# Performance work log

Measured on AMD Instinct MI355X. Metric: run time of the kernel, lower is better.

## Reference

```python
import jax, jax.numpy as jnp
import numpy as np

B, S, D = 16, 2048, 256
HEAD_SIZE = 256  # input_size // num_heads = 256 // 1
SCALE = HEAD_SIZE ** -0.5


def setup_inputs() -> dict:
    key = jax.random.key(0)
    ks = jax.random.split(key, 4)
    s = 1.0 / np.sqrt(D)  # typical linear init scale
    return {
        "x": jax.random.normal(ks[0], (B, S, D), dtype=jnp.float32),
        "Wq": jax.random.normal(ks[1], (D, D), dtype=jnp.float32) * s,
        "bq": jnp.zeros((D,), dtype=jnp.float32),
        "Wk": jax.random.normal(ks[2], (D, D), dtype=jnp.float32) * s,
        "bk": jnp.zeros((D,), dtype=jnp.float32),
        "Wv": jax.random.normal(ks[3], (D, D), dtype=jnp.float32) * s,
        "bv": jnp.zeros((D,), dtype=jnp.float32),
    }


def reference(x, Wq, bq, Wk, bk, Wv, bv):
    # Linear projections (torch Linear: x @ W.T + b)
    q = jnp.einsum("bsd,ed->bse", x, Wq) + bq
    k = jnp.einsum("bsd,ed->bse", x, Wk) + bk
    v = jnp.einsum("bsd,ed->bse", x, Wv) + bv
    # Full attention matrix [B, S, S], scaled by head_size^-0.5
    scores = jnp.einsum("bqd,bkd->bqk", q, k) * SCALE
    attn = jax.nn.softmax(scores, axis=-1)
    # dropout is identity in inference/reference mode
    out = jnp.einsum("bqk,bkd->bqd", attn, v)
    return out
```

## Files before the change

kernel.cpp:

```cpp
#include <hip/hip_runtime.h>
#include <hip/hip_bf16.h>
#include <stdint.h>

#define DEV __device__ __forceinline__

typedef __attribute__((ext_vector_type(8))) short bf16x8;
typedef __attribute__((ext_vector_type(4))) float f32x4;
typedef unsigned short u16;

DEV void gload_lds16(const void* g, void* l) {
    typedef const __attribute__((address_space(1))) unsigned int* gp_t;
    typedef __attribute__((address_space(3))) unsigned int* lp_t;
    __builtin_amdgcn_global_load_lds((gp_t)(uintptr_t)g, (lp_t)(uint32_t)(uintptr_t)l, 16, 0, 0);
}

DEV u16 f2bf(float x) {
    union { __hip_bfloat16 h; u16 u; } c;
    c.h = __float2bfloat16(x);
    return c.u;
}
DEV unsigned pack2bf(float a, float b) {
    return (unsigned)f2bf(a) | ((unsigned)f2bf(b) << 16);
}

__global__ void cast_kernel(const float* __restrict__ src, u16* __restrict__ dst, int n8) {
    int stride = gridDim.x * blockDim.x;
    for (int i = blockIdx.x * blockDim.x + threadIdx.x; i < n8; i += stride) {
        const float4* s = (const float4*)src + (size_t)i * 2;
        float4 a = s[0], b = s[1];
        union { u16 u[8]; uint4 v; } o;
        o.u[0] = f2bf(a.x); o.u[1] = f2bf(a.y); o.u[2] = f2bf(a.z); o.u[3] = f2bf(a.w);
        o.u[4] = f2bf(b.x); o.u[5] = f2bf(b.y); o.u[6] = f2bf(b.z); o.u[7] = f2bf(b.w);
        *((uint4*)dst + i) = o.v;
    }
}

DEV void gemm_body(const u16* A, const u16* Bw, const float* bias, int bias_row,
                   u16* out, int out_pitch)
{
    __shared__ char smA[16384];
    __shared__ char smB[16384];
    const int lane = threadIdx.x & 63;
    const int w    = threadIdx.x >> 6;
    const int wr   = w >> 1, wc = w & 1;
    const int l15  = lane & 15, lg = lane >> 4;

    f32x4 acc[4][4] = {};
    const char* ag = (const char*)A;
    const char* bg = (const char*)Bw;

    for (int kt = 0; kt < 4; ++kt) {
        __syncthreads();
        #pragma unroll
        for (int c = 0; c < 8; ++c) {
            int ch    = w * 8 + c;
            int loc   = ch & 15;
            int p     = loc * 1024 + lane * 16;
            int row   = p >> 7;
            int inner = (p & 127) ^ ((row & 7) << 4);
            const char* src = (ch < 16 ? ag : bg) + row * 512 + kt * 128 + inner;
            char* dst = (ch < 16 ? smA : smB) + loc * 1024;
            gload_lds16(src, dst);
        }
        __syncthreads();
        #pragma unroll
        for (int ks = 0; ks < 2; ++ks) {
            bf16x8 af[4], bfr[4];
            #pragma unroll
            for (int mi = 0; mi < 4; ++mi) {
                int row = wr * 64 + mi * 16 + l15;
                af[mi] = *(const bf16x8*)(smA + ((row * 128 + ks * 64 + lg * 16) ^ ((row & 7) << 4)));
            }
            #pragma unroll
            for (int ni = 0; ni < 4; ++ni) {
                int row = wc * 64 + ni * 16 + l15;
                bfr[ni] = *(const bf16x8*)(smB + ((row * 128 + ks * 64 + lg * 16) ^ ((row & 7) << 4)));
            }
            #pragma unroll
            for (int mi = 0; mi < 4; ++mi)
                #pragma unroll
                for (int ni = 0; ni < 4; ++ni)
                    acc[mi][ni] = __builtin_amdgcn_mfma_f32_16x16x32_bf16(af[mi], bfr[ni], acc[mi][ni], 0, 0, 0);
        }
    }
    #pragma unroll
    for (int mi = 0; mi < 4; ++mi) {
        #pragma unroll
        for (int ni = 0; ni < 4; ++ni) {
            int n_l  = wc * 64 + ni * 16 + l15;
            float bn = bias_row ? 0.f : bias[n_l];
            #pragma unroll
            for (int r = 0; r < 4; ++r) {
                int row  = wr * 64 + mi * 16 + lg * 4 + r;
                float bb = bias_row ? bias[row] : bn;
                out[(size_t)row * out_pitch + n_l] = f2bf(acc[mi][ni][r] + bb);
            }
        }
    }
}

__global__ __launch_bounds__(256) void proj_qk_kernel(
    const u16* xb, const u16* wqb, const u16* wkb,
    const float* bq, const float* bk, u16* Q, u16* K)
{
    int n0 = blockIdx.x * 128;
    int m0 = blockIdx.y * 128;
    bool isK = n0 >= 256;
    int  nl  = n0 & 255;
    gemm_body(xb + (size_t)m0 * 256, (isK ? wkb : wqb) + (size_t)nl * 256,
              (isK ? bk : bq) + nl, 0,
              (isK ? K : Q) + (size_t)m0 * 256 + nl, 256);
}

__global__ __launch_bounds__(256) void proj_v_kernel(
    const u16* wvb, const u16* xb, const float* bv, u16* Vt)
{
    int n0 = blockIdx.x * 128;
    int m0 = blockIdx.y * 128;
    gemm_body(wvb + (size_t)m0 * 256, xb + (size_t)n0 * 256, bv + m0, 1,
              Vt + (size_t)m0 * 32768 + n0, 32768);
}

__global__ __launch_bounds__(256, 2) void attn_kernel(
    const u16* __restrict__ Q, const u16* __restrict__ K,
    const u16* __restrict__ Vt, float* __restrict__ out)
{
    __shared__ char sm[65536];

    const int lane = threadIdx.x & 63;
    const int w    = threadIdx.x >> 6;
    const int l15  = lane & 15;
    const int lg   = lane >> 4;

    const int lin = blockIdx.y * 32 + blockIdx.x;
    const int b   = (lin & 7) * 2 + ((lin >> 3) & 1);
    const int qt  = lin >> 4;
    const size_t tokbase = (size_t)b * 2048;
    const int q0w = qt * 64 + w * 16;

    bf16x8 qf[8];
    {
        const char* qrow = (const char*)(Q + (tokbase + q0w + l15) * 256);
        #pragma unroll
        for (int ks = 0; ks < 8; ++ks)
            qf[ks] = *(const bf16x8*)(qrow + ks * 64 + lg * 16);
    }

    auto stage = [&](int t) {
        const int kv0 = t * 32;
        char* kb = sm + ((t & 1) << 14);
        char* vb = sm + 32768 + ((t & 1) << 14);
        if (w < 2) {
            #pragma unroll
            for (int c = 0; c < 8; ++c) {
                int ch    = w * 8 + c;
                int row   = ch * 2 + (lane >> 5);
                int inner = ((lane & 31) * 16) ^ ((row & 7) << 4);
                gload_lds16((const char*)K + (tokbase + kv0 + row) * 512 + inner,
                            kb + ch * 1024);
            }
        } else {
            #pragma unroll
            for (int c = 0; c < 8; ++c) {
                int ch    = (w - 2) * 8 + c;
                int row   = ch * 16 + (lane >> 2);
                int inner = ((lane & 3) * 16) ^ (((row >> 1) & 3) << 4);
                gload_lds16((const char*)Vt + (size_t)row * 65536 + (size_t)(tokbase + kv0) * 2 + inner,
                            vb + ch * 1024);
            }
        }
    };

    f32x4 acc[16] = {};
    float m_run = -1e30f;
    float l_lane = 0.f;
    const float C = 0.09016844005556021f;

    stage(0);
    __syncthreads();

    for (int kt = 0; kt < 64; ++kt) {
        if (kt < 63) stage(kt + 1);

        const char* kls = sm + ((kt & 1) << 14);
        const char* vls = sm + 32768 + ((kt & 1) << 14);

        f32x4 st0 = {}, st1 = {};
        #pragma unroll
        for (int ks = 0; ks < 8; ++ks) {
            int r0 = l15, r1 = 16 + l15;
            bf16x8 kf0 = *(const bf16x8*)(kls + ((r0 * 512 + ks * 64 + lg * 16) ^ ((r0 & 7) << 4)));
            bf16x8 kf1 = *(const bf16x8*)(kls + ((r1 * 512 + ks * 64 + lg * 16) ^ ((r1 & 7) << 4)));
            st0 = __builtin_amdgcn_mfma_f32_16x16x32_bf16(kf0, qf[ks], st0, 0, 0, 0);
            st1 = __builtin_amdgcn_mfma_f32_16x16x32_bf16(kf1, qf[ks], st1, 0, 0, 0);
        }

        float p0 = fmaxf(fmaxf(st0[0], st0[1]), fmaxf(st0[2], st0[3]));
        float p1 = fmaxf(fmaxf(st1[0], st1[1]), fmaxf(st1[2], st1[3]));
        float lmax = fmaxf(p0, p1);

        if (__any(lmax > m_run + 16.f)) {
            float rmax = lmax;
            rmax = fmaxf(rmax, __shfl_xor(rmax, 16, 64));
            rmax = fmaxf(rmax, __shfl_xor(rmax, 32, 64));
            float m_new = fmaxf(m_run, rmax);
            float rs = exp2f((m_run - m_new) * C);
            #pragma unroll
            for (int dt = 0; dt < 16; ++dt) acc[dt] *= rs;
            l_lane *= rs;
            m_run = m_new;
        }

        const float mc = m_run * C;
        float sum = 0.f;
        #pragma unroll
        for (int i = 0; i < 4; ++i) {
            float e0 = exp2f(st0[i] * C - mc);
            float e1 = exp2f(st1[i] * C - mc);
            st0[i] = e0; st1[i] = e1;
            sum += e0 + e1;
        }
        l_lane += sum;

        unsigned d00 = pack2bf(st0[0], st0[1]);
        unsigned d01 = pack2bf(st0[2], st0[3]);
        unsigned d10 = pack2bf(st1[0], st1[1]);
        unsigned d11 = pack2bf(st1[2], st1[3]);

        unsigned own0 = (lg & 2) ? d10 : d00;
        unsigned own1 = (lg & 2) ? d11 : d01;
        unsigned cx0  = (lg & 2) ? d00 : d10;
        unsigned cx1  = (lg & 2) ? d01 : d11;
        unsigned r16_0 = __shfl_xor(own0, 16, 64);
        unsigned r16_1 = __shfl_xor(own1, 16, 64);
        unsigned r32_0 = __shfl_xor(cx0, 32, 64);
        unsigned r32_1 = __shfl_xor(cx1, 32, 64);
        unsigned r48_0 = __shfl_xor(cx0, 48, 64);
        unsigned r48_1 = __shfl_xor(cx1, 48, 64);
        union { unsigned u[4]; bf16x8 v; } pf;
        pf.u[0] = (lg == 0) ? own0 : (lg == 1) ? r48_0 : (lg == 2) ? r32_0 : r16_0;
        pf.u[1] = (lg == 0) ? own1 : (lg == 1) ? r48_1 : (lg == 2) ? r32_1 : r16_1;
        pf.u[2] = (lg == 0) ? r16_0 : (lg == 1) ? r32_0 : (lg == 2) ? r48_0 : own0;
        pf.u[3] = (lg == 0) ? r16_1 : (lg == 1) ? r32_1 : (lg == 2) ? r48_1 : own1;

        #pragma unroll
        for (int dt = 0; dt < 16; ++dt) {
            int row = dt * 16 + l15;
            bf16x8 vf = *(const bf16x8*)(vls + ((row * 64 + lg * 16) ^ (((row >> 1) & 3) << 4)));
            acc[dt] = __builtin_amdgcn_mfma_f32_16x16x32_bf16(vf, pf.v, acc[dt], 0, 0, 0);
        }

        __syncthreads();
    }

    float l_row = l_lane;
    l_row += __shfl_xor(l_row, 16, 64);
    l_row += __shfl_xor(l_row, 32, 64);
    const float inv = 1.f / l_row;

    float* ow = (float*)(sm + w * 4352);
    #pragma unroll
    for (int p = 0; p < 4; ++p) {
        #pragma unroll
        for (int d2 = 0; d2 < 4; ++d2) {
            const int dt = p * 4 + d2;
            #pragma unroll
            for (int r = 0; r < 4; ++r)
                ow[l15 * 68 + d2 * 16 + lg * 4 + r] = acc[dt][r] * inv;
        }
        const int row = lane >> 2;
        const int c0  = (lane & 3) * 16;
        #pragma unroll
        for (int i = 0; i < 4; ++i) {
            float4 v = *(const float4*)(ow + row * 68 + c0 + i * 4);
            *(float4*)(out + (tokbase + q0w + row) * 256 + p * 64 + c0 + i * 4) = v;
        }
    }
}

extern "C" void kernel_launch(void* const* d_in, const int* in_sizes, int n_in,
                              void* d_out, int out_size, void* d_ws, size_t ws_size,
                              hipStream_t stream) {
    (void)in_sizes; (void)n_in; (void)out_size; (void)ws_size;
    const float* x  = (const float*)d_in[0];
    const float* Wq = (const float*)d_in[1];
    const float* bq = (const float*)d_in[2];
    const float* Wk = (const float*)d_in[3];
    const float* bk = (const float*)d_in[4];
    const float* Wv = (const float*)d_in[5];
    const float* bv = (const float*)d_in[6];
    float* out = (float*)d_out;

    char* ws = (char*)d_ws;
    u16* xb  = (u16*)(ws);
    u16* wqb = (u16*)(ws + 16777216);
    u16* wkb = (u16*)(ws + 16908288);
    u16* wvb = (u16*)(ws + 17039360);
    u16* Qb  = (u16*)(ws + 17170432);
    u16* Kb  = (u16*)(ws + 33947648);
    u16* Vtb = (u16*)(ws + 50724864);

    cast_kernel<<<2048, 256, 0, stream>>>(x,  xb,  1048576);
    cast_kernel<<<64,   256, 0, stream>>>(Wq, wqb, 8192);
    cast_kernel<<<64,   256, 0, stream>>>(Wk, wkb, 8192);
    cast_kernel<<<64,   256, 0, stream>>>(Wv, wvb, 8192);

    proj_qk_kernel<<<dim3(4, 256), 256, 0, stream>>>(xb, wqb, wkb, bq, bk, Qb, Kb);
    proj_v_kernel<<<dim3(256, 2), 256, 0, stream>>>(wvb, xb, bv, Vtb);

    attn_kernel<<<dim3(32, 16), 256, 0, stream>>>(Qb, Kb, Vtb, out);
}
```

Before: 166.3 us.

## Split attention KV range in two halves and merge with a combine kernel

```diff
diff --git a/kernel.cpp b/kernel.cpp
--- a/kernel.cpp
+++ b/kernel.cpp
@@ -5,6 +5,7 @@
 #define DEV __device__ __forceinline__
 
 typedef __attribute__((ext_vector_type(8))) short bf16x8;
+typedef __attribute__((ext_vector_type(4))) short bf16x4;
 typedef __attribute__((ext_vector_type(4))) float f32x4;
 typedef unsigned short u16;
 
@@ -20,8 +21,12 @@
     return c.u;
 }
 DEV unsigned pack2bf(float a, float b) {
-    return (unsigned)f2bf(a) | ((unsigned)f2bf(b) << 16);
-}
+    union { __hip_bfloat162 h2; unsigned u; } cv;
+    cv.h2 = __float22bfloat162_rn(make_float2(a, b));
+    return cv.u;
+}
+DEV float bflo(unsigned u) { union { unsigned u; float f; } c; c.u = u << 16; return c.f; }
+DEV float bfhi(unsigned u) { union { unsigned u; float f; } c; c.u = u & 0xffff0000u; return c.f; }
 
 __global__ void cast_kernel(const float* __restrict__ src, u16* __restrict__ dst, int n8) {
     int stride = gridDim.x * blockDim.x;
@@ -121,22 +126,25 @@
               Vt + (size_t)m0 * 32768 + n0, 32768);
 }
 
-__global__ __launch_bounds__(256, 2) void attn_kernel(
+__global__ __launch_bounds__(256, 4) void attn_kernel(
     const u16* __restrict__ Q, const u16* __restrict__ K,
-    const u16* __restrict__ Vt, float* __restrict__ out)
-{
-    __shared__ char sm[65536];
+    const u16* __restrict__ Vt, float* __restrict__ out,
+    u16* __restrict__ p1, float2* __restrict__ ml)
+{
+    __shared__ char sm[32768];
 
     const int lane = threadIdx.x & 63;
     const int w    = threadIdx.x >> 6;
     const int l15  = lane & 15;
     const int lg   = lane >> 4;
 
-    const int lin = blockIdx.y * 32 + blockIdx.x;
-    const int b   = (lin & 7) * 2 + ((lin >> 3) & 1);
-    const int qt  = lin >> 4;
+    const int lin  = blockIdx.x;
+    const int b    = (lin & 7) * 2 + ((lin >> 3) & 1);
+    const int half = (lin >> 4) & 1;
+    const int qt   = lin >> 5;
     const size_t tokbase = (size_t)b * 2048;
-    const int q0w = qt * 64 + w * 16;
+    const int q0w  = qt * 64 + w * 16;
+    const int kvh  = half * 1024;
 
     bf16x8 qf[8];
     {
@@ -146,59 +154,80 @@
             qf[ks] = *(const bf16x8*)(qrow + ks * 64 + lg * 16);
     }
 
-    auto stage = [&](int t) {
-        const int kv0 = t * 32;
-        char* kb = sm + ((t & 1) << 14);
-        char* vb = sm + 32768 + ((t & 1) << 14);
-        if (w < 2) {
-            #pragma unroll
-            for (int c = 0; c < 8; ++c) {
-                int ch    = w * 8 + c;
-                int row   = ch * 2 + (lane >> 5);
-                int inner = ((lane & 31) * 16) ^ ((row & 7) << 4);
-                gload_lds16((const char*)K + (tokbase + kv0 + row) * 512 + inner,
-                            kb + ch * 1024);
-            }
-        } else {
-            #pragma unroll
-            for (int c = 0; c < 8; ++c) {
-                int ch    = (w - 2) * 8 + c;
-                int row   = ch * 16 + (lane >> 2);
-                int inner = ((lane & 3) * 16) ^ (((row >> 1) & 3) << 4);
-                gload_lds16((const char*)Vt + (size_t)row * 65536 + (size_t)(tokbase + kv0) * 2 + inner,
-                            vb + ch * 1024);
-            }
-        }
-    };
+    uint32_t kgo[2];
+    {
+        int row = lane >> 2;
+        uint32_t byte = (uint32_t)((lane & 3) * 16) ^ (((row >> 1) & 3) << 4);
+        kgo[0] = (uint32_t)row * 512 + (w * 2 + 0) * 64 + byte;
+        kgo[1] = (uint32_t)row * 512 + (w * 2 + 1) * 64 + byte;
+    }
+    const char* Kg = (const char*)K + (tokbase + kvh) * 512;
+    uint32_t vgo[4];
+    {
+        #pragma unroll
+        for (int c = 0; c < 4; ++c) {
+            int cc = w * 4 + c;
+            int d  = (cc & 7) * 32 + (lane >> 1);
+            uint32_t byte = (uint32_t)((lane & 1) * 16) ^ (((d >> 2) & 1) << 4);
+            vgo[c] = (uint32_t)d * 65536 + (cc >> 3) * 32 + byte;
+        }
+    }
+    const char* Vg = (const char*)Vt + (tokbase + kvh) * 2;
+
+    const int kbase = l15 * 64 + ((lg * 16) ^ (((l15 >> 1) & 3) << 4));
+    const int vbase = l15 * 32 + ((lg * 8)  ^ (((l15 >> 2) & 1) << 4));
+    const char* k0p = sm + kbase;
+    const char* k1p = sm + 8192 + kbase;
+    const char* v0p = sm + 16384 + vbase;
+    const char* v1p = sm + 24576 + vbase;
 
     f32x4 acc[16] = {};
     float m_run = -1e30f;
     float l_lane = 0.f;
     const float C = 0.09016844005556021f;
 
-    stage(0);
+    auto stageK = [&](int t, int sel) {
+        const char* gb = Kg + (size_t)t * 8192;
+        gload_lds16(gb + kgo[0], sm + sel * 8192 + (w * 2 + 0) * 1024);
+        gload_lds16(gb + kgo[1], sm + sel * 8192 + (w * 2 + 1) * 1024);
+    };
+    auto stageV2 = [&](int t0) {
+        const char* gb = Vg + (size_t)t0 * 32;
+        #pragma unroll
+        for (int c = 0; c < 4; ++c) {
+            int cc = w * 4 + c;
+            gload_lds16(gb + vgo[c], sm + 16384 + (cc >> 3) * 8192 + (cc & 7) * 1024);
+        }
+    };
+    auto qk = [&](const char* kp) -> f32x4 {
+        f32x4 sa = {}, sb = {};
+        #pragma unroll
+        for (int ks = 0; ks < 4; ++ks) {
+            bf16x8 kf = *(const bf16x8*)(kp + ks * 1024);
+            sa = __builtin_amdgcn_mfma_f32_16x16x32_bf16(kf, qf[ks], sa, 0, 0, 0);
+        }
+        #pragma unroll
+        for (int ks = 4; ks < 8; ++ks) {
+            bf16x8 kf = *(const bf16x8*)(kp + ks * 1024);
+            sb = __builtin_amdgcn_mfma_f32_16x16x32_bf16(kf, qf[ks], sb, 0, 0, 0);
+        }
+        return sa + sb;
+    };
+
+    stageK(0, 0);
     __syncthreads();
 
-    for (int kt = 0; kt < 64; ++kt) {
-        if (kt < 63) stage(kt + 1);
-
-        const char* kls = sm + ((kt & 1) << 14);
-        const char* vls = sm + 32768 + ((kt & 1) << 14);
-
-        f32x4 st0 = {}, st1 = {};
-        #pragma unroll
-        for (int ks = 0; ks < 8; ++ks) {
-            int r0 = l15, r1 = 16 + l15;
-            bf16x8 kf0 = *(const bf16x8*)(kls + ((r0 * 512 + ks * 64 + lg * 16) ^ ((r0 & 7) << 4)));
-            bf16x8 kf1 = *(const bf16x8*)(kls + ((r1 * 512 + ks * 64 + lg * 16) ^ ((r1 & 7) << 4)));
-            st0 = __builtin_amdgcn_mfma_f32_16x16x32_bf16(kf0, qf[ks], st0, 0, 0, 0);
-            st1 = __builtin_amdgcn_mfma_f32_16x16x32_bf16(kf1, qf[ks], st1, 0, 0, 0);
-        }
-
-        float p0 = fmaxf(fmaxf(st0[0], st0[1]), fmaxf(st0[2], st0[3]));
-        float p1 = fmaxf(fmaxf(st1[0], st1[1]), fmaxf(st1[2], st1[3]));
-        float lmax = fmaxf(p0, p1);
-
+    for (int u = 0; u < 32; ++u) {
+        stageK(2 * u + 1, 1);
+        stageV2(2 * u);
+        f32x4 stA = qk(k0p);
+        __syncthreads();
+
+        if (u < 31) stageK(2 * u + 2, 0);
+        f32x4 stB = qk(k1p);
+
+        float lmax = fmaxf(fmaxf(fmaxf(stA[0], stA[1]), fmaxf(stA[2], stA[3])),
+                           fmaxf(fmaxf(stB[0], stB[1]), fmaxf(stB[2], stB[3])));
         if (__any(lmax > m_run + 16.f)) {
             float rmax = lmax;
             rmax = fmaxf(rmax, __shfl_xor(rmax, 16, 64));
@@ -210,53 +239,34 @@
             l_lane *= rs;
             m_run = m_new;
         }
-
         const float mc = m_run * C;
-        float sum = 0.f;
-        #pragma unroll
-        for (int i = 0; i < 4; ++i) {
-            float e0 = exp2f(st0[i] * C - mc);
-            float e1 = exp2f(st1[i] * C - mc);
-            st0[i] = e0; st1[i] = e1;
-            sum += e0 + e1;
-        }
-        l_lane += sum;
-
-        unsigned d00 = pack2bf(st0[0], st0[1]);
-        unsigned d01 = pack2bf(st0[2], st0[3]);
-        unsigned d10 = pack2bf(st1[0], st1[1]);
-        unsigned d11 = pack2bf(st1[2], st1[3]);
-
-        unsigned own0 = (lg & 2) ? d10 : d00;
-        unsigned own1 = (lg & 2) ? d11 : d01;
-        unsigned cx0  = (lg & 2) ? d00 : d10;
-        unsigned cx1  = (lg & 2) ? d01 : d11;
-        unsigned r16_0 = __shfl_xor(own0, 16, 64);
-        unsigned r16_1 = __shfl_xor(own1, 16, 64);
-        unsigned r32_0 = __shfl_xor(cx0, 32, 64);
-        unsigned r32_1 = __shfl_xor(cx1, 32, 64);
-        unsigned r48_0 = __shfl_xor(cx0, 48, 64);
-        unsigned r48_1 = __shfl_xor(cx1, 48, 64);
-        union { unsigned u[4]; bf16x8 v; } pf;
-        pf.u[0] = (lg == 0) ? own0 : (lg == 1) ? r48_0 : (lg == 2) ? r32_0 : r16_0;
-        pf.u[1] = (lg == 0) ? own1 : (lg == 1) ? r48_1 : (lg == 2) ? r32_1 : r16_1;
-        pf.u[2] = (lg == 0) ? r16_0 : (lg == 1) ? r32_0 : (lg == 2) ? r48_0 : own0;
-        pf.u[3] = (lg == 0) ? r16_1 : (lg == 1) ? r32_1 : (lg == 2) ? r48_1 : own1;
+        float eA0 = exp2f(stA[0] * C - mc), eA1 = exp2f(stA[1] * C - mc);
+        float eA2 = exp2f(stA[2] * C - mc), eA3 = exp2f(stA[3] * C - mc);
+        float eB0 = exp2f(stB[0] * C - mc), eB1 = exp2f(stB[1] * C - mc);
+        float eB2 = exp2f(stB[2] * C - mc), eB3 = exp2f(stB[3] * C - mc);
+        l_lane += (eA0 + eA1 + eA2 + eA3) + (eB0 + eB1 + eB2 + eB3);
+
+        union { unsigned u2[2]; bf16x4 v; } pA, pB;
+        pA.u2[0] = pack2bf(eA0, eA1); pA.u2[1] = pack2bf(eA2, eA3);
+        pB.u2[0] = pack2bf(eB0, eB1); pB.u2[1] = pack2bf(eB2, eB3);
 
         #pragma unroll
         for (int dt = 0; dt < 16; ++dt) {
-            int row = dt * 16 + l15;
-            bf16x8 vf = *(const bf16x8*)(vls + ((row * 64 + lg * 16) ^ (((row >> 1) & 3) << 4)));
-            acc[dt] = __builtin_amdgcn_mfma_f32_16x16x32_bf16(vf, pf.v, acc[dt], 0, 0, 0);
-        }
-
+            bf16x4 va = *(const bf16x4*)(v0p + dt * 512);
+            bf16x4 vb = *(const bf16x4*)(v1p + dt * 512);
+            asm("v_mfma_f32_16x16x16_bf16 %0, %1, %2, %0"
+                : "+v"(acc[dt]) : "v"(va), "v"(pA.v));
+            asm("v_mfma_f32_16x16x16_bf16 %0, %1, %2, %0"
+                : "+v"(acc[dt]) : "v"(vb), "v"(pB.v));
+        }
         __syncthreads();
     }
 
     float l_row = l_lane;
     l_row += __shfl_xor(l_row, 16, 64);
     l_row += __shfl_xor(l_row, 32, 64);
-    const float inv = 1.f / l_row;
+    if (lg == 0)
+        ml[half * 32768 + (int)tokbase + q0w + l15] = make_float2(m_run, l_row);
 
     float* ow = (float*)(sm + w * 4352);
     #pragma unroll
@@ -266,16 +276,58 @@
             const int dt = p * 4 + d2;
             #pragma unroll
             for (int r = 0; r < 4; ++r)
-                ow[l15 * 68 + d2 * 16 + lg * 4 + r] = acc[dt][r] * inv;
+                ow[l15 * 68 + d2 * 16 + lg * 4 + r] = acc[dt][r];
         }
         const int row = lane >> 2;
         const int c0  = (lane & 3) * 16;
-        #pragma unroll
-        for (int i = 0; i < 4; ++i) {
-            float4 v = *(const float4*)(ow + row * 68 + c0 + i * 4);
-            *(float4*)(out + (tokbase + q0w + row) * 256 + p * 64 + c0 + i * 4) = v;
-        }
-    }
+        if (half == 0) {
+            #pragma unroll
+            for (int i = 0; i < 4; ++i) {
+                float4 v = *(const float4*)(ow + row * 68 + c0 + i * 4);
+                *(float4*)(out + (tokbase + q0w + row) * 256 + p * 64 + c0 + i * 4) = v;
+            }
+        } else {
+            #pragma unroll
+            for (int i = 0; i < 4; ++i) {
+                float4 v = *(const float4*)(ow + row * 68 + c0 + i * 4);
+                uint2 pk2 = make_uint2(pack2bf(v.x, v.y), pack2bf(v.z, v.w));
+                *(uint2*)(p1 + (tokbase + q0w + row) * 256 + p * 64 + c0 + i * 4) = pk2;
+            }
+        }
+    }
+}
+
+__global__ __launch_bounds__(256) void combine_kernel(
+    float* __restrict__ out, const u16* __restrict__ p1,
+    const float2* __restrict__ ml)
+{
+    const float C = 0.09016844005556021f;
+    int idx = blockIdx.x * 256 + threadIdx.x;
+    int q = idx >> 5;
+    int c = idx & 31;
+    float2 h0 = ml[q];
+    float2 h1 = ml[32768 + q];
+    float M  = fmaxf(h0.x, h1.x);
+    float k0 = exp2f((h0.x - M) * C);
+    float k1 = exp2f((h1.x - M) * C);
+    float inv = 1.f / (h0.y * k0 + h1.y * k1);
+    k0 *= inv; k1 *= inv;
+    size_t off = (size_t)q * 256 + c * 8;
+    float4 a0 = *(const float4*)(out + off);
+    float4 a1 = *(const float4*)(out + off + 4);
+    uint2 u0 = *(const uint2*)(p1 + off);
+    uint2 u1 = *(const uint2*)(p1 + off + 4);
+    float4 r0, r1;
+    r0.x = a0.x * k0 + bflo(u0.x) * k1;
+    r0.y = a0.y * k0 + bfhi(u0.x) * k1;
+    r0.z = a0.z * k0 + bflo(u0.y) * k1;
+    r0.w = a0.w * k0 + bfhi(u0.y) * k1;
+    r1.x = a1.x * k0 + bflo(u1.x) * k1;
+    r1.y = a1.y * k0 + bfhi(u1.x) * k1;
+    r1.z = a1.z * k0 + bflo(u1.y) * k1;
+    r1.w = a1.w * k0 + bfhi(u1.y) * k1;
+    *(float4*)(out + off)     = r0;
+    *(float4*)(out + off + 4) = r1;
 }
 
 extern "C" void kernel_launch(void* const* d_in, const int* in_sizes, int n_in,
@@ -299,6 +351,7 @@
     u16* Qb  = (u16*)(ws + 17170432);
     u16* Kb  = (u16*)(ws + 33947648);
     u16* Vtb = (u16*)(ws + 50724864);
+    float2* ml = (float2*)(ws + 67502080);
 
     cast_kernel<<<2048, 256, 0, stream>>>(x,  xb,  1048576);
     cast_kernel<<<64,   256, 0, stream>>>(Wq, wqb, 8192);
@@ -308,5 +361,6 @@
     proj_qk_kernel<<<dim3(4, 256), 256, 0, stream>>>(xb, wqb, wkb, bq, bk, Qb, Kb);
     proj_v_kernel<<<dim3(256, 2), 256, 0, stream>>>(wvb, xb, bv, Vtb);
 
-    attn_kernel<<<dim3(32, 16), 256, 0, stream>>>(Qb, Kb, Vtb, out);
-}
+    attn_kernel<<<1024, 256, 0, stream>>>(Qb, Kb, Vtb, out, xb, ml);
+    combine_kernel<<<4096, 256, 0, stream>>>(out, xb, ml);
+}
```

Result: slower. 195.2 us (+17.4%).
